# Kernel tuning notes

Measured on AMD Instinct MI355X. Metric: run time of the kernel, lower is better.

The kernel has to match this reference:

```python
import jax, jax.numpy as jnp
import numpy as np

E = 16        # num_experts
TOPK = 2      # num_experts_per_tok


def setup_inputs() -> dict:
    key = jax.random.key(0)
    ks = jax.random.split(key, 8)
    B, S, H, I, IS = 4, 2048, 1024, 512, 2048
    std = 0.02
    return {
        "hidden_states": jax.random.normal(ks[0], (B, S, H), jnp.float32),
        "gate_w": jax.random.normal(ks[1], (E, H), jnp.float32) * std,
        "gate_up_proj": jax.random.normal(ks[2], (E, 2 * I, H), jnp.float32) * std,
        "down_proj": jax.random.normal(ks[3], (E, H, I), jnp.float32) * std,
        "shared_gate_proj": jax.random.normal(ks[4], (IS, H), jnp.float32) * std,
        "shared_up_proj": jax.random.normal(ks[5], (IS, H), jnp.float32) * std,
        "shared_down_proj": jax.random.normal(ks[6], (H, IS), jnp.float32) * std,
        "shared_expert_gate_w": jax.random.normal(ks[7], (1, H), jnp.float32) * std,
    }


def _moe(x, gate_w, gate_up_proj, down_proj, sgp, sup, sdp, segw):
    # x: [N, H] flattened tokens
    N = x.shape[0]
    router_logits = x @ gate_w.T                      # [N, E]
    probs = jax.nn.softmax(router_logits, axis=-1)
    routing_weights, selected = jax.lax.top_k(probs, TOPK)   # [N, TOPK]
    routing_weights = routing_weights / routing_weights.sum(-1, keepdims=True)
    # combine weights scattered into dense [N, E] (per-token per-expert gate)
    combine = jnp.zeros((N, E), x.dtype).at[jnp.arange(N)[:, None], selected].add(routing_weights)

    def body(acc, ws):
        gu_w, d_w, cw = ws                            # [2I,H], [H,I], [N]
        gu = x @ gu_w.T                               # [N, 2I]
        g, u = jnp.split(gu, 2, axis=-1)
        h = jax.nn.silu(g) * u                        # [N, I]
        return acc + cw[:, None] * (h @ d_w.T), None

    expert_out, _ = jax.lax.scan(body, jnp.zeros_like(x), (gate_up_proj, down_proj, combine.T))

    # shared expert with sigmoid token gate
    shared_h = jax.nn.silu(x @ sgp.T) * (x @ sup.T)   # [N, IS]
    shared_out = (shared_h @ sdp.T) * jax.nn.sigmoid(x @ segw.T)  # [N, H]
    out = expert_out + shared_out

    # aux (load-balancing) loss
    counts = jnp.sum(jax.nn.one_hot(selected, E, dtype=x.dtype), axis=(0, 1))  # [E]
    frac_tokens = counts / (N * TOPK)
    frac_probs = probs.sum(0) / N
    aux_loss = E * jnp.sum(frac_tokens * frac_probs)
    return out, aux_loss


def reference(hidden_states, gate_w, gate_up_proj, down_proj, shared_gate_proj, shared_up_proj, shared_down_proj, shared_expert_gate_w):
    B, S, H = hidden_states.shape
    out, aux = _moe(hidden_states.reshape(-1, H), gate_w, gate_up_proj, down_proj,
                    shared_gate_proj, shared_up_proj, shared_down_proj, shared_expert_gate_w)
    return out.reshape(B, S, H), aux
```

## Files before the change

### kernel.cpp

```cpp
#include <hip/hip_runtime.h>
#include <hip/hip_bf16.h>
#include <stdint.h>


#define N_TOK 8192
#define HDIM 1024
#define NEXP 16
#define IEXP 512
#define ISH 2048

typedef __bf16 bf16x8 __attribute__((ext_vector_type(8)));
typedef float f32x4 __attribute__((ext_vector_type(4)));

#define OFF_XBF   ((size_t)0)
#define OFF_WSG   ((size_t)16777216)
#define OFF_WSU   ((size_t)20971520)
#define OFF_WSD   ((size_t)25165824)
#define OFF_SH    ((size_t)29360128)
#define OFF_HEXP  ((size_t)62914560)
#define OFF_IDS   ((size_t)79691776)
#define OFF_META  ((size_t)80216064)
#define OFF_SIG   ((size_t)80216320)
#define OFF_LG    ((size_t)80249088)
#define OFF_SLOT  ((size_t)81297664)
#define OFF_TWAB  ((size_t)81363200)

static __device__ __forceinline__ unsigned short f2bf(float f) {
  unsigned int u = __float_as_uint(f);
  u += 0x7fffu + ((u >> 16) & 1u);
  return (unsigned short)(u >> 16);
}
static __device__ __forceinline__ int pack_bf2(float a, float b) {
  return (int)f2bf(a) | ((int)f2bf(b) << 16);
}
static __device__ __forceinline__ float bf2f(unsigned short u) {
  return __uint_as_float(((unsigned int)u) << 16);
}
static __device__ __forceinline__ void gl_lds16(const void* g, void* l) {
  __builtin_amdgcn_global_load_lds(
      (const __attribute__((address_space(1))) unsigned int*)g,
      (__attribute__((address_space(3))) unsigned int*)l, 16, 0, 0);
}

__global__ void cvt_kernel(const float* __restrict__ src,
                           unsigned short* __restrict__ dst, int n4) {
  int i = blockIdx.x * 256 + threadIdx.x;
  if (i >= n4) return;
  float4 v = ((const float4*)src)[i];
  uint2 o;
  o.x = (unsigned)pack_bf2(v.x, v.y);
  o.y = (unsigned)pack_bf2(v.z, v.w);
  ((uint2*)dst)[i] = o;
}

__global__ __launch_bounds__(256) void logits_kernel(
    const float* __restrict__ X, const float* __restrict__ GW,
    const float* __restrict__ SEGW, float* __restrict__ LG,
    unsigned short* __restrict__ XBF) {
  int wid = threadIdx.x >> 6, lane = threadIdx.x & 63;
  int tok = blockIdx.x * 4 + wid;
  const float* xr = X + (size_t)tok * HDIM;
  unsigned short* xw = XBF + (size_t)tok * HDIM;
  float xv[16];
#pragma unroll
  for (int i = 0; i < 16; i++) xv[i] = xr[lane + 64 * i];
#pragma unroll
  for (int i = 0; i < 16; i++) xw[lane + 64 * i] = f2bf(xv[i]);
  float myv = 0.f;
#pragma unroll
  for (int e = 0; e < 17; e++) {
    const float* wr = (e < 16) ? (GW + (size_t)e * HDIM) : SEGW;
    float p = 0.f;
#pragma unroll
    for (int i = 0; i < 16; i++) p += xv[i] * wr[lane + 64 * i];
#pragma unroll
    for (int off = 32; off >= 1; off >>= 1) p += __shfl_xor(p, off, 64);
    if (lane == e) myv = p;
  }
  if (lane < 17) LG[(size_t)tok * 32 + lane] = myv;
}

__global__ __launch_bounds__(256) void route_kernel(
    const float* __restrict__ LG, int* __restrict__ cnt,
    float* __restrict__ pps, int* __restrict__ ids,
    int* __restrict__ slotAB, float* __restrict__ twAB,
    float* __restrict__ sig) {
  __shared__ int lcnt[16];
  __shared__ int lbase[16];
  __shared__ float lps[16];
  int tid = threadIdx.x;
  int tok = blockIdx.x * 256 + tid;
  if (tid < 16) { lcnt[tid] = 0; lps[tid] = 0.f; }
  __syncthreads();
  const float4* row = (const float4*)(LG + (size_t)tok * 32);
  float4 v0 = row[0], v1 = row[1], v2 = row[2], v3 = row[3];
  float g16 = row[4].x;
  float lg[16] = {v0.x, v0.y, v0.z, v0.w, v1.x, v1.y, v1.z, v1.w,
                  v2.x, v2.y, v2.z, v2.w, v3.x, v3.y, v3.z, v3.w};
  float mx = lg[0];
#pragma unroll
  for (int e = 1; e < 16; e++) mx = fmaxf(mx, lg[e]);
  float pr[16], s = 0.f;
#pragma unroll
  for (int e = 0; e < 16; e++) { pr[e] = __expf(lg[e] - mx); s += pr[e]; }
  float inv_s = 1.f / s;
  float p1 = -1.f, p2 = -1.f; int i1 = 0, i2 = 0;
#pragma unroll
  for (int e = 0; e < 16; e++) {
    if (pr[e] > p1) { p2 = p1; i2 = i1; p1 = pr[e]; i1 = e; }
    else if (pr[e] > p2) { p2 = pr[e]; i2 = e; }
  }
  float wsum = p1 + p2;
  int s1 = atomicAdd(&lcnt[i1], 1);
  int s2 = atomicAdd(&lcnt[i2], 1);
#pragma unroll
  for (int e = 0; e < 16; e++) atomicAdd(&lps[e], pr[e] * inv_s);
  sig[tok] = 1.f / (1.f + __expf(-g16));
  __syncthreads();
  if (tid < 16) {
    lbase[tid] = atomicAdd(&cnt[tid], lcnt[tid]);
    atomicAdd(&pps[tid], lps[tid]);
  }
  __syncthreads();
  int sl1 = lbase[i1] + s1, sl2 = lbase[i2] + s2;
  ids[i1 * N_TOK + sl1] = tok;
  ids[i2 * N_TOK + sl2] = tok;
  slotAB[tok * 2]     = (i1 << 14) | sl1;
  slotAB[tok * 2 + 1] = (i2 << 14) | sl2;
  twAB[tok * 2]     = p1 / wsum;
  twAB[tok * 2 + 1] = p2 / wsum;
}

__global__ void offs_aux_kernel(const int* __restrict__ cnt, int* __restrict__ off,
                                const float* __restrict__ probs_sum,
                                float* __restrict__ out_aux) {
  if (threadIdx.x == 0 && blockIdx.x == 0) {
    int run = 0; float aux = 0.f;
    for (int e = 0; e < NEXP; e++) {
      off[e] = run; run += cnt[e];
      aux += ((float)cnt[e] / (float)(N_TOK * 2)) * (probs_sum[e] / (float)N_TOK);
    }
    off[16] = run;
    *out_aux = (float)NEXP * aux;
  }
}

__global__ __launch_bounds__(256) void shared_gemm1_kernel(
    const unsigned short* __restrict__ X, const unsigned short* __restrict__ Wg,
    const unsigned short* __restrict__ Wu, unsigned short* __restrict__ H) {
  __shared__ __align__(16) unsigned short As[128 * 32];
  __shared__ __align__(16) unsigned short Bs1[64 * 32];
  __shared__ __align__(16) unsigned short Bs2[64 * 32];
  int m0 = blockIdx.y * 128, n0 = blockIdx.x * 64;
  int t = threadIdx.x, lane = t & 63, w = t >> 6;
  int wm = (w & 1) * 64, wn = (w >> 1) * 32;
  int arow = t >> 2, akb = (t & 3) * 8;
  const unsigned short* ap0 = X + (size_t)(m0 + arow) * HDIM + akb;
  const unsigned short* ap1 = X + (size_t)(m0 + 64 + arow) * HDIM + akb;
  const unsigned short* bp1 = Wg + (size_t)(n0 + arow) * HDIM + akb;
  const unsigned short* bp2 = Wu + (size_t)(n0 + arow) * HDIM + akb;
  f32x4 z = {0.f, 0.f, 0.f, 0.f};
  f32x4 accg[4][2], accu[4][2];
#pragma unroll
  for (int i = 0; i < 4; i++)
#pragma unroll
    for (int j = 0; j < 2; j++) { accg[i][j] = z; accu[i][j] = z; }
  for (int k0 = 0; k0 < HDIM; k0 += 32) {
    __syncthreads();
    gl_lds16(ap0 + k0, &As[t * 8]);
    gl_lds16(ap1 + k0, &As[2048 + t * 8]);
    gl_lds16(bp1 + k0, &Bs1[t * 8]);
    gl_lds16(bp2 + k0, &Bs2[t * 8]);
    __syncthreads();
    int fr = lane & 15, fc = (lane >> 4) * 8;
    bf16x8 af[4], bg[2], bu[2];
#pragma unroll
    for (int i = 0; i < 4; i++) af[i] = *(const bf16x8*)&As[(wm + i * 16 + fr) * 32 + fc];
#pragma unroll
    for (int j = 0; j < 2; j++) {
      bg[j] = *(const bf16x8*)&Bs1[(wn + j * 16 + fr) * 32 + fc];
      bu[j] = *(const bf16x8*)&Bs2[(wn + j * 16 + fr) * 32 + fc];
    }
#pragma unroll
    for (int i = 0; i < 4; i++)
#pragma unroll
      for (int j = 0; j < 2; j++) {
        accg[i][j] = __builtin_amdgcn_mfma_f32_16x16x32_bf16(af[i], bg[j], accg[i][j], 0, 0, 0);
        accu[i][j] = __builtin_amdgcn_mfma_f32_16x16x32_bf16(af[i], bu[j], accu[i][j], 0, 0, 0);
      }
  }
  int col = lane & 15, rq = (lane >> 4) * 4;
#pragma unroll
  for (int i = 0; i < 4; i++)
#pragma unroll
    for (int j = 0; j < 2; j++)
#pragma unroll
      for (int r = 0; r < 4; r++) {
        int mm = m0 + wm + i * 16 + rq + r;
        int nn = n0 + wn + j * 16 + col;
        float g = accg[i][j][r], u = accu[i][j][r];
        float h = g / (1.f + __expf(-g)) * u;
        H[(size_t)mm * ISH + nn] = f2bf(h);
      }
}

__global__ __launch_bounds__(256) void shared_gemm2_kernel(
    const unsigned short* __restrict__ H, const unsigned short* __restrict__ Wd,
    const float* __restrict__ sig, float* __restrict__ Out) {
  __shared__ __align__(16) unsigned short As[128 * 32];
  __shared__ __align__(16) unsigned short Bs[128 * 32];
  int m0 = blockIdx.y * 128, n0 = blockIdx.x * 128;
  int t = threadIdx.x, lane = t & 63, w = t >> 6;
  int wm = (w & 1) * 64, wn = (w >> 1) * 64;
  int arow = t >> 2, akb = (t & 3) * 8;
  const unsigned short* apA0 = H + (size_t)(m0 + arow) * ISH + akb;
  const unsigned short* apA1 = H + (size_t)(m0 + 64 + arow) * ISH + akb;
  const unsigned short* apB0 = Wd + (size_t)(n0 + arow) * ISH + akb;
  const unsigned short* apB1 = Wd + (size_t)(n0 + 64 + arow) * ISH + akb;
  f32x4 z = {0.f, 0.f, 0.f, 0.f};
  f32x4 acc[4][4];
#pragma unroll
  for (int i = 0; i < 4; i++)
#pragma unroll
    for (int j = 0; j < 4; j++) acc[i][j] = z;
  for (int k0 = 0; k0 < ISH; k0 += 32) {
    __syncthreads();
    gl_lds16(apA0 + k0, &As[t * 8]);
    gl_lds16(apA1 + k0, &As[2048 + t * 8]);
    gl_lds16(apB0 + k0, &Bs[t * 8]);
    gl_lds16(apB1 + k0, &Bs[2048 + t * 8]);
    __syncthreads();
    int fr = lane & 15, fc = (lane >> 4) * 8;
    bf16x8 af[4], bfr[4];
#pragma unroll
    for (int i = 0; i < 4; i++) {
      af[i] = *(const bf16x8*)&As[(wm + i * 16 + fr) * 32 + fc];
      bfr[i] = *(const bf16x8*)&Bs[(wn + i * 16 + fr) * 32 + fc];
    }
#pragma unroll
    for (int i = 0; i < 4; i++)
#pragma unroll
      for (int j = 0; j < 4; j++)
        acc[i][j] = __builtin_amdgcn_mfma_f32_16x16x32_bf16(af[i], bfr[j], acc[i][j], 0, 0, 0);
  }
  int col = lane & 15, rq = (lane >> 4) * 4;
#pragma unroll
  for (int i = 0; i < 4; i++)
#pragma unroll
    for (int r = 0; r < 4; r++) {
      int mm = m0 + wm + i * 16 + rq + r;
      float sg = sig[mm];
#pragma unroll
      for (int j = 0; j < 4; j++) {
        int nn = n0 + wn + j * 16 + col;
        Out[(size_t)mm * HDIM + nn] = acc[i][j][r] * sg;
      }
    }
}

__global__ __launch_bounds__(256) void exp_gemm1_kernel(
    const unsigned short* __restrict__ X, const unsigned short* __restrict__ WGUb,
    const int* __restrict__ ids, const int* __restrict__ cnt,
    const int* __restrict__ off, unsigned short* __restrict__ Hexp) {
  int e = blockIdx.z;
  int ne = cnt[e];
  int m0 = blockIdx.y * 128;
  if (m0 >= ne) return;
  __shared__ __align__(16) unsigned short As[128 * 32];
  __shared__ __align__(16) unsigned short Bs1[64 * 32];
  __shared__ __align__(16) unsigned short Bs2[64 * 32];
  int n0 = blockIdx.x * 64;
  const int* eids = ids + e * N_TOK;
  int base = off[e];
  int t = threadIdx.x, lane = t & 63, w = t >> 6;
  int wm = (w & 1) * 64, wn = (w >> 1) * 32;
  int arow = t >> 2, akb = (t & 3) * 8;
  int s0 = m0 + arow, s1 = m0 + 64 + arow;
  int t0 = (s0 < ne) ? eids[s0] : 0;
  int t1 = (s1 < ne) ? eids[s1] : 0;
  const unsigned short* ap0 = X + (size_t)t0 * HDIM + akb;
  const unsigned short* ap1 = X + (size_t)t1 * HDIM + akb;
  const unsigned short* bpg = WGUb + ((size_t)e * 1024 + n0 + arow) * HDIM + akb;
  const unsigned short* bpu = WGUb + ((size_t)e * 1024 + 512 + n0 + arow) * HDIM + akb;
  f32x4 z = {0.f, 0.f, 0.f, 0.f};
  f32x4 accg[4][2], accu[4][2];
#pragma unroll
  for (int i = 0; i < 4; i++)
#pragma unroll
    for (int j = 0; j < 2; j++) { accg[i][j] = z; accu[i][j] = z; }
  for (int k0 = 0; k0 < HDIM; k0 += 32) {
    __syncthreads();
    gl_lds16(ap0 + k0, &As[t * 8]);
    gl_lds16(ap1 + k0, &As[2048 + t * 8]);
    gl_lds16(bpg + k0, &Bs1[t * 8]);
    gl_lds16(bpu + k0, &Bs2[t * 8]);
    __syncthreads();
    int fr = lane & 15, fc = (lane >> 4) * 8;
    bf16x8 af[4], bg[2], bu[2];
#pragma unroll
    for (int i = 0; i < 4; i++) af[i] = *(const bf16x8*)&As[(wm + i * 16 + fr) * 32 + fc];
#pragma unroll
    for (int j = 0; j < 2; j++) {
      bg[j] = *(const bf16x8*)&Bs1[(wn + j * 16 + fr) * 32 + fc];
      bu[j] = *(const bf16x8*)&Bs2[(wn + j * 16 + fr) * 32 + fc];
    }
#pragma unroll
    for (int i = 0; i < 4; i++)
#pragma unroll
      for (int j = 0; j < 2; j++) {
        accg[i][j] = __builtin_amdgcn_mfma_f32_16x16x32_bf16(af[i], bg[j], accg[i][j], 0, 0, 0);
        accu[i][j] = __builtin_amdgcn_mfma_f32_16x16x32_bf16(af[i], bu[j], accu[i][j], 0, 0, 0);
      }
  }
  int col = lane & 15, rq = (lane >> 4) * 4;
#pragma unroll
  for (int i = 0; i < 4; i++)
#pragma unroll
    for (int j = 0; j < 2; j++)
#pragma unroll
      for (int r = 0; r < 4; r++) {
        int slot = m0 + wm + i * 16 + rq + r;
        if (slot < ne) {
          int nn = n0 + wn + j * 16 + col;
          float g = accg[i][j][r], u = accu[i][j][r];
          float h = g / (1.f + __expf(-g)) * u;
          Hexp[(size_t)(base + slot) * IEXP + nn] = f2bf(h);
        }
      }
}

__global__ __launch_bounds__(256) void exp_gemm2_kernel(
    const unsigned short* __restrict__ Hexp, const unsigned short* __restrict__ WDb,
    const int* __restrict__ cnt, const int* __restrict__ off,
    unsigned short* __restrict__ Eout) {
  int e = blockIdx.z;
  int ne = cnt[e];
  int m0 = blockIdx.y * 128;
  if (m0 >= ne) return;
  __shared__ __align__(16) unsigned short As[128 * 32];
  __shared__ __align__(16) unsigned short Bs[128 * 32];
  int n0 = blockIdx.x * 128;
  int base = off[e];
  int t = threadIdx.x, lane = t & 63, w = t >> 6;
  int wm = (w & 1) * 64, wn = (w >> 1) * 64;
  int arow = t >> 2, akb = (t & 3) * 8;
  int ra0 = base + m0 + arow;        if (ra0 > 16383) ra0 = 16383;
  int ra1 = base + m0 + 64 + arow;   if (ra1 > 16383) ra1 = 16383;
  const unsigned short* ap0 = Hexp + (size_t)ra0 * IEXP + akb;
  const unsigned short* ap1 = Hexp + (size_t)ra1 * IEXP + akb;
  const unsigned short* bp0 = WDb + ((size_t)e * HDIM + n0 + arow) * IEXP + akb;
  const unsigned short* bp1 = WDb + ((size_t)e * HDIM + n0 + 64 + arow) * IEXP + akb;
  f32x4 z = {0.f, 0.f, 0.f, 0.f};
  f32x4 acc[4][4];
#pragma unroll
  for (int i = 0; i < 4; i++)
#pragma unroll
    for (int j = 0; j < 4; j++) acc[i][j] = z;
  for (int k0 = 0; k0 < IEXP; k0 += 32) {
    __syncthreads();
    gl_lds16(ap0 + k0, &As[t * 8]);
    gl_lds16(ap1 + k0, &As[2048 + t * 8]);
    gl_lds16(bp0 + k0, &Bs[t * 8]);
    gl_lds16(bp1 + k0, &Bs[2048 + t * 8]);
    __syncthreads();
    int fr = lane & 15, fc = (lane >> 4) * 8;
    bf16x8 af[4], bfr[4];
#pragma unroll
    for (int i = 0; i < 4; i++) {
      af[i] = *(const bf16x8*)&As[(wm + i * 16 + fr) * 32 + fc];
      bfr[i] = *(const bf16x8*)&Bs[(wn + i * 16 + fr) * 32 + fc];
    }
#pragma unroll
    for (int i = 0; i < 4; i++)
#pragma unroll
      for (int j = 0; j < 4; j++)
        acc[i][j] = __builtin_amdgcn_mfma_f32_16x16x32_bf16(af[i], bfr[j], acc[i][j], 0, 0, 0);
  }
  int col = lane & 15, rq = (lane >> 4) * 4;
#pragma unroll
  for (int i = 0; i < 4; i++)
#pragma unroll
    for (int r = 0; r < 4; r++) {
      int slot = m0 + wm + i * 16 + rq + r;
      if (slot < ne) {
#pragma unroll
        for (int j = 0; j < 4; j++) {
          int nn = n0 + wn + j * 16 + col;
          Eout[(size_t)(base + slot) * HDIM + nn] = f2bf(acc[i][j][r]);
        }
      }
    }
}

__global__ __launch_bounds__(256) void combine_kernel(
    const unsigned short* __restrict__ Eout, const int* __restrict__ slotAB,
    const float* __restrict__ twAB, const int* __restrict__ off,
    float* __restrict__ Out) {
  int tok = blockIdx.x, t = threadIdx.x;
  int sa = slotAB[tok * 2], sb = slotAB[tok * 2 + 1];
  float wa = twAB[tok * 2], wb = twAB[tok * 2 + 1];
  int ra = off[sa >> 14] + (sa & 16383);
  int rb = off[sb >> 14] + (sb & 16383);
  const ushort4 a4 = *(const ushort4*)(Eout + (size_t)ra * HDIM + t * 4);
  const ushort4 b4 = *(const ushort4*)(Eout + (size_t)rb * HDIM + t * 4);
  float* po = Out + (size_t)tok * HDIM + t * 4;
  float4 o = *(const float4*)po;
  o.x += wa * bf2f(a4.x) + wb * bf2f(b4.x);
  o.y += wa * bf2f(a4.y) + wb * bf2f(b4.y);
  o.z += wa * bf2f(a4.z) + wb * bf2f(b4.z);
  o.w += wa * bf2f(a4.w) + wb * bf2f(b4.w);
  *(float4*)po = o;
}

extern "C" void kernel_launch(void* const* d_in, const int* in_sizes, int n_in,
                              void* d_out, int out_size, void* d_ws, size_t ws_size,
                              hipStream_t stream) {
  const float* X   = (const float*)d_in[0];
  const float* GW  = (const float*)d_in[1];
  const float* WGU = (const float*)d_in[2];
  const float* WDN = (const float*)d_in[3];
  const float* WSG = (const float*)d_in[4];
  const float* WSU = (const float*)d_in[5];
  const float* WSD = (const float*)d_in[6];
  const float* SEGW = (const float*)d_in[7];
  float* Out = (float*)d_out;
  char* ws = (char*)d_ws;

  unsigned short* xbf  = (unsigned short*)(ws + OFF_XBF);
  unsigned short* wsg  = (unsigned short*)(ws + OFF_WSG);
  unsigned short* wsu  = (unsigned short*)(ws + OFF_WSU);
  unsigned short* wsd  = (unsigned short*)(ws + OFF_WSD);
  unsigned short* sh   = (unsigned short*)(ws + OFF_SH);
  unsigned short* hexp = (unsigned short*)(ws + OFF_HEXP);
  int*   ids  = (int*)(ws + OFF_IDS);
  int*   cnt  = (int*)(ws + OFF_META);
  int*   off  = (int*)(ws + OFF_META + 64);
  float* pps  = (float*)(ws + OFF_META + 144);
  float* sig  = (float*)(ws + OFF_SIG);
  float* lg   = (float*)(ws + OFF_LG);
  int*   slotAB = (int*)(ws + OFF_SLOT);
  float* twAB   = (float*)(ws + OFF_TWAB);
  unsigned short* wgu_bf = (unsigned short*)(ws + OFF_SH);
  unsigned short* wdn_bf = (unsigned short*)(ws + OFF_XBF);
  unsigned short* eout   = (unsigned short*)(ws + OFF_SH);

  hipMemsetAsync(ws + OFF_META, 0, 256, stream);

  {
    int n4;
    n4 = (ISH * HDIM) / 4;
    cvt_kernel<<<(n4 + 255) / 256, 256, 0, stream>>>(WSG, wsg, n4);
    cvt_kernel<<<(n4 + 255) / 256, 256, 0, stream>>>(WSU, wsu, n4);
    n4 = (HDIM * ISH) / 4;
    cvt_kernel<<<(n4 + 255) / 256, 256, 0, stream>>>(WSD, wsd, n4);
  }

  logits_kernel<<<N_TOK / 4, 256, 0, stream>>>(X, GW, SEGW, lg, xbf);
  route_kernel<<<N_TOK / 256, 256, 0, stream>>>(lg, cnt, pps, ids, slotAB, twAB, sig);
  offs_aux_kernel<<<1, 64, 0, stream>>>(cnt, off, pps, Out + (size_t)N_TOK * HDIM);

  shared_gemm1_kernel<<<dim3(ISH / 64, N_TOK / 128), 256, 0, stream>>>(xbf, wsg, wsu, sh);
  shared_gemm2_kernel<<<dim3(HDIM / 128, N_TOK / 128), 256, 0, stream>>>(sh, wsd, sig, Out);

  {
    int n4 = (NEXP * 2 * IEXP * HDIM) / 4;
    cvt_kernel<<<(n4 + 255) / 256, 256, 0, stream>>>(WGU, wgu_bf, n4);
  }
  exp_gemm1_kernel<<<dim3(IEXP / 64, N_TOK / 128, NEXP), 256, 0, stream>>>(
      xbf, wgu_bf, ids, cnt, off, hexp);
  {
    int n4 = (NEXP * HDIM * IEXP) / 4;
    cvt_kernel<<<(n4 + 255) / 256, 256, 0, stream>>>(WDN, wdn_bf, n4);
  }
  exp_gemm2_kernel<<<dim3(HDIM / 128, N_TOK / 128, NEXP), 256, 0, stream>>>(
      hexp, wdn_bf, cnt, off, eout);
  combine_kernel<<<N_TOK, 256, 0, stream>>>(eout, slotAB, twAB, off, Out);
}
```

Before: 495.1 us.

## Replace shared-gate and expert GEMMs with 256x256 double-buffered 8-wave pipelined kernel

Introduces a templated gemm8p kernel with 256x256 tiles, 512 threads, 128KB dynamic LDS double buffering, XOR-swizzled LDS layout and a four-phase schedule that interleaves global-to-LDS prefetch with MFMA work using barriers and setprio. It replaces shared_gemm1, exp_gemm1 and exp_gemm2, interleaving gate/up columns so SiLU*up fuses in the epilogue, and uses a grid-stride loop over token tiles for experts. The aim is to raise MFMA utilisation and hide load latency versus the simple single-buffered 128-tile kernels. The risks are the heavy LDS use, which limits occupancy, and load imbalance across experts with uneven token counts.

```diff
diff --git a/kernel.cpp b/kernel.cpp
--- a/kernel.cpp
+++ b/kernel.cpp
@@ -145,63 +145,226 @@
   }
 }
 
-__global__ __launch_bounds__(256) void shared_gemm1_kernel(
-    const unsigned short* __restrict__ X, const unsigned short* __restrict__ Wg,
-    const unsigned short* __restrict__ Wu, unsigned short* __restrict__ H) {
-  __shared__ __align__(16) unsigned short As[128 * 32];
-  __shared__ __align__(16) unsigned short Bs1[64 * 32];
-  __shared__ __align__(16) unsigned short Bs2[64 * 32];
-  int m0 = blockIdx.y * 128, n0 = blockIdx.x * 64;
-  int t = threadIdx.x, lane = t & 63, w = t >> 6;
-  int wm = (w & 1) * 64, wn = (w >> 1) * 32;
-  int arow = t >> 2, akb = (t & 3) * 8;
-  const unsigned short* ap0 = X + (size_t)(m0 + arow) * HDIM + akb;
-  const unsigned short* ap1 = X + (size_t)(m0 + 64 + arow) * HDIM + akb;
-  const unsigned short* bp1 = Wg + (size_t)(n0 + arow) * HDIM + akb;
-  const unsigned short* bp2 = Wu + (size_t)(n0 + arow) * HDIM + akb;
-  f32x4 z = {0.f, 0.f, 0.f, 0.f};
-  f32x4 accg[4][2], accu[4][2];
-#pragma unroll
-  for (int i = 0; i < 4; i++)
-#pragma unroll
-    for (int j = 0; j < 2; j++) { accg[i][j] = z; accu[i][j] = z; }
-  for (int k0 = 0; k0 < HDIM; k0 += 32) {
-    __syncthreads();
-    gl_lds16(ap0 + k0, &As[t * 8]);
-    gl_lds16(ap1 + k0, &As[2048 + t * 8]);
-    gl_lds16(bp1 + k0, &Bs1[t * 8]);
-    gl_lds16(bp2 + k0, &Bs2[t * 8]);
-    __syncthreads();
-    int fr = lane & 15, fc = (lane >> 4) * 8;
-    bf16x8 af[4], bg[2], bu[2];
-#pragma unroll
-    for (int i = 0; i < 4; i++) af[i] = *(const bf16x8*)&As[(wm + i * 16 + fr) * 32 + fc];
-#pragma unroll
-    for (int j = 0; j < 2; j++) {
-      bg[j] = *(const bf16x8*)&Bs1[(wn + j * 16 + fr) * 32 + fc];
-      bu[j] = *(const bf16x8*)&Bs2[(wn + j * 16 + fr) * 32 + fc];
+template <int MODE>
+__global__ __launch_bounds__(512, 2) void gemm8p_kernel(
+    const unsigned short* __restrict__ A,
+    const unsigned short* __restrict__ B1,
+    const unsigned short* __restrict__ B2,
+    const int* __restrict__ ids, const int* __restrict__ cnt,
+    const int* __restrict__ off, unsigned short* __restrict__ Out) {
+  constexpr int KD = (MODE == 2) ? IEXP : HDIM;
+  constexpr int NK = KD / 64;
+  extern __shared__ unsigned short lds[];
+
+  int ne, base, e;
+  if constexpr (MODE == 0) { e = 0; ne = N_TOK; base = 0; }
+  else { e = blockIdx.z; ne = cnt[e]; base = off[e]; }
+
+  const int t = threadIdx.x, lane = t & 63, w = t >> 6;
+  const int fr = lane & 15, hi = lane >> 4;
+  const int rq = hi * 4;
+  const int Rm = (w >> 2) * 64;
+  const int wn = (w & 3) * 32;
+  const int srow = t >> 3;
+  const int sblk = t & 7;
+  const int cb = (sblk ^ (srow & 7)) * 8;
+  const int s0 = ((0 + hi) ^ (fr & 7)) * 8;
+  const int s1 = ((4 + hi) ^ (fr & 7)) * 8;
+  const f32x4 z = {0.f, 0.f, 0.f, 0.f};
+
+#define STG_A(buf, h, kt)                                                     \
+  do {                                                                        \
+    gl_lds16(apt[h][0] + (kt) * 64, &lds[(buf)*32768 + (h)*8192 + t * 8]);    \
+    gl_lds16(apt[h][1] + (kt) * 64,                                           \
+             &lds[(buf)*32768 + (h)*8192 + 4096 + t * 8]);                    \
+  } while (0)
+#define STG_B(buf, h, kt)                                                     \
+  do {                                                                        \
+    gl_lds16(bpt[h][0] + (kt) * 64,                                           \
+             &lds[(buf)*32768 + 16384 + (h)*8192 + t * 8]);                   \
+    gl_lds16(bpt[h][1] + (kt) * 64,                                           \
+             &lds[(buf)*32768 + 16384 + (h)*8192 + 4096 + t * 8]);            \
+  } while (0)
+
+  for (int m0 = blockIdx.y * 256; m0 < ne; m0 += gridDim.y * 256) {
+    const unsigned short* apt[2][2];
+    const unsigned short* bpt[2][2];
+#pragma unroll
+    for (int h = 0; h < 2; h++)
+#pragma unroll
+      for (int l = 0; l < 2; l++) {
+        int r = h * 128 + l * 64 + srow;
+        int arow;
+        if constexpr (MODE == 0) {
+          arow = m0 + r;
+        } else if constexpr (MODE == 1) {
+          int slot = m0 + r;
+          arow = (slot < ne) ? ids[e * N_TOK + slot] : 0;
+        } else {
+          int ra = base + m0 + r;
+          if (ra > 16383) ra = 16383;
+          arow = ra;
+        }
+        apt[h][l] = A + (size_t)arow * KD + cb;
+        if constexpr (MODE == 0) {
+          int gcol = blockIdx.x * 128 + ((r >> 5) << 4) + (r & 15);
+          const unsigned short* W = (r & 16) ? B2 : B1;
+          bpt[h][l] = W + (size_t)gcol * HDIM + cb;
+        } else if constexpr (MODE == 1) {
+          int wrow = ((r & 16) ? 512 : 0) + blockIdx.x * 128 + ((r >> 5) << 4) + (r & 15);
+          bpt[h][l] = B1 + ((size_t)e * 1024 + wrow) * HDIM + cb;
+        } else {
+          int nrow = blockIdx.x * 256 + r;
+          bpt[h][l] = B1 + ((size_t)e * HDIM + nrow) * IEXP + cb;
+        }
+      }
+
+    f32x4 acc[8][4];
+#pragma unroll
+    for (int i = 0; i < 8; i++)
+#pragma unroll
+      for (int j = 0; j < 4; j++) acc[i][j] = z;
+
+    STG_A(0, 0, 0); STG_B(0, 1, 0); STG_A(0, 1, 0); STG_B(0, 0, 0);
+    if (NK > 1) {
+      STG_A(1, 0, 1); STG_B(1, 1, 1);
+      asm volatile("s_waitcnt vmcnt(4)" ::: "memory");
+    } else {
+      asm volatile("s_waitcnt vmcnt(0)" ::: "memory");
     }
-#pragma unroll
-    for (int i = 0; i < 4; i++)
+    __builtin_amdgcn_s_barrier();
+
+    for (int kt = 0; kt < NK; ++kt) {
+      const int c = kt & 1, nb = c ^ 1;
+      const unsigned short* Ab = &lds[c * 32768];
+      const unsigned short* Bb = &lds[c * 32768 + 16384];
+      bf16x8 a[4][2], b[2][2];
+
+#pragma unroll
+      for (int i = 0; i < 4; i++) {
+        int ro = (Rm + i * 16 + fr) * 64;
+        a[i][0] = *(const bf16x8*)&Ab[ro + s0];
+        a[i][1] = *(const bf16x8*)&Ab[ro + s1];
+      }
 #pragma unroll
       for (int j = 0; j < 2; j++) {
-        accg[i][j] = __builtin_amdgcn_mfma_f32_16x16x32_bf16(af[i], bg[j], accg[i][j], 0, 0, 0);
-        accu[i][j] = __builtin_amdgcn_mfma_f32_16x16x32_bf16(af[i], bu[j], accu[i][j], 0, 0, 0);
-      }
-  }
-  int col = lane & 15, rq = (lane >> 4) * 4;
-#pragma unroll
-  for (int i = 0; i < 4; i++)
-#pragma unroll
-    for (int j = 0; j < 2; j++)
-#pragma unroll
-      for (int r = 0; r < 4; r++) {
-        int mm = m0 + wm + i * 16 + rq + r;
-        int nn = n0 + wn + j * 16 + col;
-        float g = accg[i][j][r], u = accu[i][j][r];
-        float h = g / (1.f + __expf(-g)) * u;
-        H[(size_t)mm * ISH + nn] = f2bf(h);
-      }
+        int ro = (wn + j * 16 + fr) * 64;
+        b[j][0] = *(const bf16x8*)&Bb[ro + s0];
+        b[j][1] = *(const bf16x8*)&Bb[ro + s1];
+      }
+      if (kt + 1 < NK) STG_A(nb, 1, kt + 1);
+      __builtin_amdgcn_s_barrier();
+      asm volatile("s_waitcnt lgkmcnt(0)" ::: "memory");
+      __builtin_amdgcn_s_setprio(1);
+#pragma unroll
+      for (int i = 0; i < 4; i++)
+#pragma unroll
+        for (int j = 0; j < 2; j++) {
+          acc[i][j] = __builtin_amdgcn_mfma_f32_16x16x32_bf16(a[i][0], b[j][0], acc[i][j], 0, 0, 0);
+          acc[i][j] = __builtin_amdgcn_mfma_f32_16x16x32_bf16(a[i][1], b[j][1], acc[i][j], 0, 0, 0);
+        }
+      __builtin_amdgcn_s_setprio(0);
+      __builtin_amdgcn_s_barrier();
+
+#pragma unroll
+      for (int j = 0; j < 2; j++) {
+        int ro = (128 + wn + j * 16 + fr) * 64;
+        b[j][0] = *(const bf16x8*)&Bb[ro + s0];
+        b[j][1] = *(const bf16x8*)&Bb[ro + s1];
+      }
+      if (kt + 1 < NK) STG_B(nb, 0, kt + 1);
+      __builtin_amdgcn_s_barrier();
+      asm volatile("s_waitcnt lgkmcnt(0)" ::: "memory");
+      __builtin_amdgcn_s_setprio(1);
+#pragma unroll
+      for (int i = 0; i < 4; i++)
+#pragma unroll
+        for (int j = 0; j < 2; j++) {
+          acc[i][2 + j] = __builtin_amdgcn_mfma_f32_16x16x32_bf16(a[i][0], b[j][0], acc[i][2 + j], 0, 0, 0);
+          acc[i][2 + j] = __builtin_amdgcn_mfma_f32_16x16x32_bf16(a[i][1], b[j][1], acc[i][2 + j], 0, 0, 0);
+        }
+      __builtin_amdgcn_s_setprio(0);
+      __builtin_amdgcn_s_barrier();
+
+#pragma unroll
+      for (int i = 0; i < 4; i++) {
+        int ro = (128 + Rm + i * 16 + fr) * 64;
+        a[i][0] = *(const bf16x8*)&Ab[ro + s0];
+        a[i][1] = *(const bf16x8*)&Ab[ro + s1];
+      }
+      if (kt + 2 < NK) STG_A(c, 0, kt + 2);
+      __builtin_amdgcn_s_barrier();
+      asm volatile("s_waitcnt lgkmcnt(0)" ::: "memory");
+      __builtin_amdgcn_s_setprio(1);
+#pragma unroll
+      for (int i = 0; i < 4; i++)
+#pragma unroll
+        for (int j = 0; j < 2; j++) {
+          acc[4 + i][2 + j] = __builtin_amdgcn_mfma_f32_16x16x32_bf16(a[i][0], b[j][0], acc[4 + i][2 + j], 0, 0, 0);
+          acc[4 + i][2 + j] = __builtin_amdgcn_mfma_f32_16x16x32_bf16(a[i][1], b[j][1], acc[4 + i][2 + j], 0, 0, 0);
+        }
+      __builtin_amdgcn_s_setprio(0);
+      __builtin_amdgcn_s_barrier();
+
+#pragma unroll
+      for (int j = 0; j < 2; j++) {
+        int ro = (wn + j * 16 + fr) * 64;
+        b[j][0] = *(const bf16x8*)&Bb[ro + s0];
+        b[j][1] = *(const bf16x8*)&Bb[ro + s1];
+      }
+      if (kt + 2 < NK) STG_B(c, 1, kt + 2);
+      __builtin_amdgcn_s_barrier();
+      asm volatile("s_waitcnt lgkmcnt(0)" ::: "memory");
+      __builtin_amdgcn_s_setprio(1);
+#pragma unroll
+      for (int i = 0; i < 4; i++)
+#pragma unroll
+        for (int j = 0; j < 2; j++) {
+          acc[4 + i][j] = __builtin_amdgcn_mfma_f32_16x16x32_bf16(a[i][0], b[j][0], acc[4 + i][j], 0, 0, 0);
+          acc[4 + i][j] = __builtin_amdgcn_mfma_f32_16x16x32_bf16(a[i][1], b[j][1], acc[4 + i][j], 0, 0, 0);
+        }
+      __builtin_amdgcn_s_setprio(0);
+      if (kt + 2 < NK) asm volatile("s_waitcnt vmcnt(4)" ::: "memory");
+      else             asm volatile("s_waitcnt vmcnt(0)" ::: "memory");
+      __builtin_amdgcn_s_barrier();
+    }
+
+#pragma unroll
+    for (int i = 0; i < 8; i++) {
+      int mloc = (i >> 2) * 128 + Rm + (i & 3) * 16 + rq;
+      if constexpr (MODE == 2) {
+#pragma unroll
+        for (int j = 0; j < 4; j++) {
+          int nn = blockIdx.x * 256 + (j >> 1) * 128 + wn + (j & 1) * 16 + fr;
+#pragma unroll
+          for (int r = 0; r < 4; r++) {
+            int slot = m0 + mloc + r;
+            if (slot < ne)
+              Out[(size_t)(base + slot) * HDIM + nn] = f2bf(acc[i][j][r]);
+          }
+        }
+      } else {
+#pragma unroll
+        for (int p = 0; p < 2; p++) {
+          int cc = blockIdx.x * 128 + p * 64 + (w & 3) * 16 + fr;
+#pragma unroll
+          for (int r = 0; r < 4; r++) {
+            int slot = m0 + mloc + r;
+            float g = acc[i][2 * p][r], u = acc[i][2 * p + 1][r];
+            float hv = g / (1.f + __expf(-g)) * u;
+            if constexpr (MODE == 0) {
+              Out[(size_t)slot * ISH + cc] = f2bf(hv);
+            } else {
+              if (slot < ne)
+                Out[(size_t)(base + slot) * IEXP + cc] = f2bf(hv);
+            }
+          }
+        }
+      }
+    }
+  }
+#undef STG_A
+#undef STG_B
 }
 
 __global__ __launch_bounds__(256) void shared_gemm2_kernel(
@@ -254,140 +417,6 @@
       for (int j = 0; j < 4; j++) {
         int nn = n0 + wn + j * 16 + col;
         Out[(size_t)mm * HDIM + nn] = acc[i][j][r] * sg;
-      }
-    }
-}
-
-__global__ __launch_bounds__(256) void exp_gemm1_kernel(
-    const unsigned short* __restrict__ X, const unsigned short* __restrict__ WGUb,
-    const int* __restrict__ ids, const int* __restrict__ cnt,
-    const int* __restrict__ off, unsigned short* __restrict__ Hexp) {
-  int e = blockIdx.z;
-  int ne = cnt[e];
-  int m0 = blockIdx.y * 128;
-  if (m0 >= ne) return;
-  __shared__ __align__(16) unsigned short As[128 * 32];
-  __shared__ __align__(16) unsigned short Bs1[64 * 32];
-  __shared__ __align__(16) unsigned short Bs2[64 * 32];
-  int n0 = blockIdx.x * 64;
-  const int* eids = ids + e * N_TOK;
-  int base = off[e];
-  int t = threadIdx.x, lane = t & 63, w = t >> 6;
-  int wm = (w & 1) * 64, wn = (w >> 1) * 32;
-  int arow = t >> 2, akb = (t & 3) * 8;
-  int s0 = m0 + arow, s1 = m0 + 64 + arow;
-  int t0 = (s0 < ne) ? eids[s0] : 0;
-  int t1 = (s1 < ne) ? eids[s1] : 0;
-  const unsigned short* ap0 = X + (size_t)t0 * HDIM + akb;
-  const unsigned short* ap1 = X + (size_t)t1 * HDIM + akb;
-  const unsigned short* bpg = WGUb + ((size_t)e * 1024 + n0 + arow) * HDIM + akb;
-  const unsigned short* bpu = WGUb + ((size_t)e * 1024 + 512 + n0 + arow) * HDIM + akb;
-  f32x4 z = {0.f, 0.f, 0.f, 0.f};
-  f32x4 accg[4][2], accu[4][2];
-#pragma unroll
-  for (int i = 0; i < 4; i++)
-#pragma unroll
-    for (int j = 0; j < 2; j++) { accg[i][j] = z; accu[i][j] = z; }
-  for (int k0 = 0; k0 < HDIM; k0 += 32) {
-    __syncthreads();
-    gl_lds16(ap0 + k0, &As[t * 8]);
-    gl_lds16(ap1 + k0, &As[2048 + t * 8]);
-    gl_lds16(bpg + k0, &Bs1[t * 8]);
-    gl_lds16(bpu + k0, &Bs2[t * 8]);
-    __syncthreads();
-    int fr = lane & 15, fc = (lane >> 4) * 8;
-    bf16x8 af[4], bg[2], bu[2];
-#pragma unroll
-    for (int i = 0; i < 4; i++) af[i] = *(const bf16x8*)&As[(wm + i * 16 + fr) * 32 + fc];
-#pragma unroll
-    for (int j = 0; j < 2; j++) {
-      bg[j] = *(const bf16x8*)&Bs1[(wn + j * 16 + fr) * 32 + fc];
-      bu[j] = *(const bf16x8*)&Bs2[(wn + j * 16 + fr) * 32 + fc];
-    }
-#pragma unroll
-    for (int i = 0; i < 4; i++)
-#pragma unroll
-      for (int j = 0; j < 2; j++) {
-        accg[i][j] = __builtin_amdgcn_mfma_f32_16x16x32_bf16(af[i], bg[j], accg[i][j], 0, 0, 0);
-        accu[i][j] = __builtin_amdgcn_mfma_f32_16x16x32_bf16(af[i], bu[j], accu[i][j], 0, 0, 0);
-      }
-  }
-  int col = lane & 15, rq = (lane >> 4) * 4;
-#pragma unroll
-  for (int i = 0; i < 4; i++)
-#pragma unroll
-    for (int j = 0; j < 2; j++)
-#pragma unroll
-      for (int r = 0; r < 4; r++) {
-        int slot = m0 + wm + i * 16 + rq + r;
-        if (slot < ne) {
-          int nn = n0 + wn + j * 16 + col;
-          float g = accg[i][j][r], u = accu[i][j][r];
-          float h = g / (1.f + __expf(-g)) * u;
-          Hexp[(size_t)(base + slot) * IEXP + nn] = f2bf(h);
-        }
-      }
-}
-
-__global__ __launch_bounds__(256) void exp_gemm2_kernel(
-    const unsigned short* __restrict__ Hexp, const unsigned short* __restrict__ WDb,
-    const int* __restrict__ cnt, const int* __restrict__ off,
-    unsigned short* __restrict__ Eout) {
-  int e = blockIdx.z;
-  int ne = cnt[e];
-  int m0 = blockIdx.y * 128;
-  if (m0 >= ne) return;
-  __shared__ __align__(16) unsigned short As[128 * 32];
-  __shared__ __align__(16) unsigned short Bs[128 * 32];
-  int n0 = blockIdx.x * 128;
-  int base = off[e];
-  int t = threadIdx.x, lane = t & 63, w = t >> 6;
-  int wm = (w & 1) * 64, wn = (w >> 1) * 64;
-  int arow = t >> 2, akb = (t & 3) * 8;
-  int ra0 = base + m0 + arow;        if (ra0 > 16383) ra0 = 16383;
-  int ra1 = base + m0 + 64 + arow;   if (ra1 > 16383) ra1 = 16383;
-  const unsigned short* ap0 = Hexp + (size_t)ra0 * IEXP + akb;
-  const unsigned short* ap1 = Hexp + (size_t)ra1 * IEXP + akb;
-  const unsigned short* bp0 = WDb + ((size_t)e * HDIM + n0 + arow) * IEXP + akb;
-  const unsigned short* bp1 = WDb + ((size_t)e * HDIM + n0 + 64 + arow) * IEXP + akb;
-  f32x4 z = {0.f, 0.f, 0.f, 0.f};
-  f32x4 acc[4][4];
-#pragma unroll
-  for (int i = 0; i < 4; i++)
-#pragma unroll
-    for (int j = 0; j < 4; j++) acc[i][j] = z;
-  for (int k0 = 0; k0 < IEXP; k0 += 32) {
-    __syncthreads();
-    gl_lds16(ap0 + k0, &As[t * 8]);
-    gl_lds16(ap1 + k0, &As[2048 + t * 8]);
-    gl_lds16(bp0 + k0, &Bs[t * 8]);
-    gl_lds16(bp1 + k0, &Bs[2048 + t * 8]);
-    __syncthreads();
-    int fr = lane & 15, fc = (lane >> 4) * 8;
-    bf16x8 af[4], bfr[4];
-#pragma unroll
-    for (int i = 0; i < 4; i++) {
-      af[i] = *(const bf16x8*)&As[(wm + i * 16 + fr) * 32 + fc];
-      bfr[i] = *(const bf16x8*)&Bs[(wn + i * 16 + fr) * 32 + fc];
-    }
-#pragma unroll
-    for (int i = 0; i < 4; i++)
-#pragma unroll
-      for (int j = 0; j < 4; j++)
-        acc[i][j] = __builtin_amdgcn_mfma_f32_16x16x32_bf16(af[i], bfr[j], acc[i][j], 0, 0, 0);
-  }
-  int col = lane & 15, rq = (lane >> 4) * 4;
-#pragma unroll
-  for (int i = 0; i < 4; i++)
-#pragma unroll
-    for (int r = 0; r < 4; r++) {
-      int slot = m0 + wm + i * 16 + rq + r;
-      if (slot < ne) {
-#pragma unroll
-        for (int j = 0; j < 4; j++) {
-          int nn = n0 + wn + j * 16 + col;
-          Eout[(size_t)(base + slot) * HDIM + nn] = f2bf(acc[i][j][r]);
-        }
       }
     }
 }
@@ -444,6 +473,13 @@
   unsigned short* wdn_bf = (unsigned short*)(ws + OFF_XBF);
   unsigned short* eout   = (unsigned short*)(ws + OFF_SH);
 
+  (void)hipFuncSetAttribute((const void*)gemm8p_kernel<0>,
+                            hipFuncAttributeMaxDynamicSharedMemorySize, 131072);
+  (void)hipFuncSetAttribute((const void*)gemm8p_kernel<1>,
+                            hipFuncAttributeMaxDynamicSharedMemorySize, 131072);
+  (void)hipFuncSetAttribute((const void*)gemm8p_kernel<2>,
+                            hipFuncAttributeMaxDynamicSharedMemorySize, 131072);
+
   hipMemsetAsync(ws + OFF_META, 0, 256, stream);
 
   {
@@ -459,20 +495,21 @@
   route_kernel<<<N_TOK / 256, 256, 0, stream>>>(lg, cnt, pps, ids, slotAB, twAB, sig);
   offs_aux_kernel<<<1, 64, 0, stream>>>(cnt, off, pps, Out + (size_t)N_TOK * HDIM);
 
-  shared_gemm1_kernel<<<dim3(ISH / 64, N_TOK / 128), 256, 0, stream>>>(xbf, wsg, wsu, sh);
+  gemm8p_kernel<0><<<dim3(ISH * 2 / 256, N_TOK / 256), 512, 131072, stream>>>(
+      xbf, wsg, wsu, ids, cnt, off, sh);
   shared_gemm2_kernel<<<dim3(HDIM / 128, N_TOK / 128), 256, 0, stream>>>(sh, wsd, sig, Out);
 
   {
     int n4 = (NEXP * 2 * IEXP * HDIM) / 4;
     cvt_kernel<<<(n4 + 255) / 256, 256, 0, stream>>>(WGU, wgu_bf, n4);
   }
-  exp_gemm1_kernel<<<dim3(IEXP / 64, N_TOK / 128, NEXP), 256, 0, stream>>>(
-      xbf, wgu_bf, ids, cnt, off, hexp);
+  gemm8p_kernel<1><<<dim3(IEXP * 2 / 256, 8, NEXP), 512, 131072, stream>>>(
+      xbf, wgu_bf, wgu_bf, ids, cnt, off, hexp);
   {
     int n4 = (NEXP * HDIM * IEXP) / 4;
     cvt_kernel<<<(n4 + 255) / 256, 256, 0, stream>>>(WDN, wdn_bf, n4);
   }
-  exp_gemm2_kernel<<<dim3(HDIM / 128, N_TOK / 128, NEXP), 256, 0, stream>>>(
-      hexp, wdn_bf, cnt, off, eout);
+  gemm8p_kernel<2><<<dim3(HDIM / 256, 8, NEXP), 512, 131072, stream>>>(
+      hexp, wdn_bf, wdn_bf, ids, cnt, off, eout);
   combine_kernel<<<N_TOK, 256, 0, stream>>>(eout, slotAB, twAB, off, Out);
 }
```

New measurement: 507.7 us. 1.03x slower.
